# Optimization experiments

Measured on AMD Instinct MI355X. Metric: run time of the kernel, lower is better.

The kernel has to match this reference:

```python
import jax, jax.numpy as jnp
import numpy as np
import math

B, L, H, D, V, N = 16, 2048, 768, 64, 32128, 20


def setup_inputs() -> dict:
    key = jax.random.key(0)
    ks = jax.random.split(key, 10)
    f = lambda k, shape, s: jax.random.normal(k, shape, dtype=jnp.float32) * s
    return {
        "relevance": jax.random.uniform(ks[0], (B,), dtype=jnp.float32),
        "input_ids": jax.random.randint(ks[1], (B, L), 0, V),
        "wte_weight": f(ks[2], (V, H), 0.02),
        "prompts": f(ks[3], (N, H), 1.0),
        "label_prompts": f(ks[4], (2, H), 1.0),
        "aq_w": f(ks[5], (D, H), 0.02), "aq_b": jnp.zeros((D,), jnp.float32),
        "ak_w": f(ks[6], (D, H), 0.02), "ak_b": jnp.zeros((D,), jnp.float32),
        "lq_w": f(ks[7], (D, H), 0.02), "lq_b": jnp.zeros((D,), jnp.float32),
        "lk_w": f(ks[8], (D, H), 0.02), "lk_b": jnp.zeros((D,), jnp.float32),
    }


def _adapter(hidden, prompts, qw, qb, kw, kb):
    # InstanceWisePrompt: mean_L(Q K^T) == Q @ mean_L(K) (exact linearity of mean)
    Q = prompts @ qw.T + qb                    # (N, d)
    K_mean = (hidden @ kw.T + kb).mean(axis=1)  # (B, d)
    scores = jnp.einsum('nd,bd->bn', Q, K_mean) / math.sqrt(Q.shape[-1])  # (B, N)
    probs = jax.nn.sigmoid(scores)
    return prompts[None, :, :] * probs[:, :, None]  # (B, N, H)


def reference(relevance, input_ids, wte_weight, prompts, label_prompts,
              aq_w, aq_b, ak_w, ak_b, lq_w, lq_b, lk_w, lk_b):
    hs_src = wte_weight[input_ids]                       # (B, L, H) embedding gather
    rel2 = jnp.stack([1.0 - relevance, relevance], 1)    # (B, 2)
    hs_rel = (rel2 @ label_prompts)[:, None, :]          # (B, 1, H)
    lbl_prompts = _adapter(hs_rel, prompts, lq_w, lq_b, lk_w, lk_b)  # (B, N, H)
    doc_prompts = _adapter(hs_src, prompts, aq_w, aq_b, ak_w, ak_b)  # (B, N, H)
    return jnp.concatenate([lbl_prompts, doc_prompts, hs_src], axis=1)  # (B, 2N+L, H)
```

## Files before the change

kernel.cpp:

```cpp
#include <hip/hip_runtime.h>
#include <math.h>

namespace {
constexpr int B = 16, L = 2048, H = 768, D = 64, N = 20;
constexpr int TOK = 2 * N + L;
constexpr int ROWS = 16;
constexpr int NQ = N * D;
constexpr int NK = B * D;
constexpr int NQK = 2 * NQ + 2 * NK;
constexpr int WS_HSUM = 0;
constexpr int WS_QK = B * H;
constexpr int WS_PL = WS_QK + NQK;
constexpr int WS_PA = WS_PL + B * N;
}

__global__ __launch_bounds__(192) void gather_kernel(
    const int* __restrict__ ids, const float* __restrict__ wte,
    float* __restrict__ out, float* __restrict__ hsum)
{
    const int blk = blockIdx.x;
    const int b = blk / (L / ROWS);
    const int l0 = (blk % (L / ROWS)) * ROWS;
    const int t = threadIdx.x;
    float4 acc = make_float4(0.f, 0.f, 0.f, 0.f);
    float* outb = out + (size_t)b * TOK * H + (size_t)(2 * N + l0) * H;
#pragma unroll 4
    for (int r = 0; r < ROWS; ++r) {
        const int idx = ids[b * L + l0 + r];
        const float4 v = *reinterpret_cast<const float4*>(wte + (size_t)idx * H + 4 * t);
        acc.x += v.x; acc.y += v.y; acc.z += v.z; acc.w += v.w;
        *reinterpret_cast<float4*>(outb + (size_t)r * H + 4 * t) = v;
    }
    float* hs = hsum + b * H + 4 * t;
    atomicAdd(hs + 0, acc.x);
    atomicAdd(hs + 1, acc.y);
    atomicAdd(hs + 2, acc.z);
    atomicAdd(hs + 3, acc.w);
}

__global__ __launch_bounds__(256) void qk_kernel(
    const float* __restrict__ relevance, const float* __restrict__ prompts,
    const float* __restrict__ label_prompts,
    const float* __restrict__ aq_w, const float* __restrict__ aq_b,
    const float* __restrict__ ak_w, const float* __restrict__ ak_b,
    const float* __restrict__ lq_w, const float* __restrict__ lq_b,
    const float* __restrict__ lk_w, const float* __restrict__ lk_b,
    const float* __restrict__ hsum, float* __restrict__ qk)
{
    const int wave = (blockIdx.x * 256 + threadIdx.x) >> 6;
    const int lane = threadIdx.x & 63;
    if (wave >= NQK) return;

    float s = 0.f;
    float bias = 0.f;
    if (wave < NQ) {
        const int n = wave / D, d = wave % D;
        const float* x = prompts + n * H;
        const float* w = lq_w + d * H;
        for (int h = lane; h < H; h += 64) s += x[h] * w[h];
        bias = lq_b[d];
    } else if (wave < 2 * NQ) {
        const int e = wave - NQ;
        const int n = e / D, d = e % D;
        const float* x = prompts + n * H;
        const float* w = aq_w + d * H;
        for (int h = lane; h < H; h += 64) s += x[h] * w[h];
        bias = aq_b[d];
    } else if (wave < 2 * NQ + NK) {
        const int e = wave - 2 * NQ;
        const int b = e / D, d = e % D;
        const float r = relevance[b];
        const float* w = lk_w + d * H;
        for (int h = lane; h < H; h += 64) {
            const float hr = (1.f - r) * label_prompts[h] + r * label_prompts[H + h];
            s += hr * w[h];
        }
        bias = lk_b[d];
    } else {
        const int e = wave - 2 * NQ - NK;
        const int b = e / D, d = e % D;
        const float* x = hsum + b * H;
        const float* w = ak_w + d * H;
        const float inv_l = 1.f / (float)L;
        for (int h = lane; h < H; h += 64) s += (x[h] * inv_l) * w[h];
        bias = ak_b[d];
    }
#pragma unroll
    for (int off = 32; off > 0; off >>= 1) s += __shfl_xor(s, off);
    if (lane == 0) qk[wave] = s + bias;
}

__global__ __launch_bounds__(64) void score_kernel(
    const float* __restrict__ qk, float* __restrict__ probs_l,
    float* __restrict__ probs_a)
{
    const int t = blockIdx.x * 64 + threadIdx.x;
    if (t >= 2 * B * N) return;
    const int seg = t / (B * N);
    const int r = t % (B * N);
    const int b = r / N, n = r % N;
    const float* Q = qk + (seg ? NQ : 0) + n * D;
    const float* K = qk + 2 * NQ + (seg ? NK : 0) + b * D;
    float s = 0.f;
#pragma unroll
    for (int d = 0; d < D; ++d) s += Q[d] * K[d];
    s *= 0.125f;
    const float p = 1.f / (1.f + expf(-s));
    (seg ? probs_a : probs_l)[r] = p;
}

__global__ __launch_bounds__(192) void prompt_out_kernel(
    const float* __restrict__ prompts, const float* __restrict__ probs_l,
    const float* __restrict__ probs_a, float* __restrict__ out)
{
    const int blk = blockIdx.x;
    const int b = blk / (2 * N);
    const int sn = blk % (2 * N);
    const int seg = sn / N;
    const int n = sn % N;
    const float p = seg ? probs_a[b * N + n] : probs_l[b * N + n];
    const int t = threadIdx.x;
    float4 v = *reinterpret_cast<const float4*>(prompts + n * H + 4 * t);
    v.x *= p; v.y *= p; v.z *= p; v.w *= p;
    *reinterpret_cast<float4*>(out + (size_t)b * TOK * H + (size_t)sn * H + 4 * t) = v;
}

extern "C" void kernel_launch(void* const* d_in, const int* in_sizes, int n_in,
                              void* d_out, int out_size, void* d_ws, size_t ws_size,
                              hipStream_t stream)
{
    const float* relevance     = (const float*)d_in[0];
    const int*   input_ids     = (const int*)d_in[1];
    const float* wte_weight    = (const float*)d_in[2];
    const float* prompts       = (const float*)d_in[3];
    const float* label_prompts = (const float*)d_in[4];
    const float* aq_w = (const float*)d_in[5];
    const float* aq_b = (const float*)d_in[6];
    const float* ak_w = (const float*)d_in[7];
    const float* ak_b = (const float*)d_in[8];
    const float* lq_w = (const float*)d_in[9];
    const float* lq_b = (const float*)d_in[10];
    const float* lk_w = (const float*)d_in[11];
    const float* lk_b = (const float*)d_in[12];
    float* out = (float*)d_out;

    float* ws      = (float*)d_ws;
    float* hsum    = ws + WS_HSUM;
    float* qk      = ws + WS_QK;
    float* probs_l = ws + WS_PL;
    float* probs_a = ws + WS_PA;

    hipMemsetAsync(hsum, 0, B * H * sizeof(float), stream);

    gather_kernel<<<B * L / ROWS, 192, 0, stream>>>(input_ids, wte_weight, out, hsum);
    qk_kernel<<<(NQK * 64 + 255) / 256, 256, 0, stream>>>(
        relevance, prompts, label_prompts, aq_w, aq_b, ak_w, ak_b,
        lq_w, lq_b, lk_w, lk_b, hsum, qk);
    score_kernel<<<(2 * B * N + 63) / 64, 64, 0, stream>>>(qk, probs_l, probs_a);
    prompt_out_kernel<<<B * 2 * N, 192, 0, stream>>>(prompts, probs_l, probs_a, out);
}
```

Before: 236.0 us.

## Replace atomic row-sum accumulation with per-block partials and a reduce kernel

```diff
diff --git a/kernel.cpp b/kernel.cpp
--- a/kernel.cpp
+++ b/kernel.cpp
@@ -5,22 +5,25 @@
 constexpr int B = 16, L = 2048, H = 768, D = 64, N = 20;
 constexpr int TOK = 2 * N + L;
 constexpr int ROWS = 16;
+constexpr int BLK_PER_B = L / ROWS;
+constexpr int NBLK = B * BLK_PER_B;
 constexpr int NQ = N * D;
 constexpr int NK = B * D;
 constexpr int NQK = 2 * NQ + 2 * NK;
-constexpr int WS_HSUM = 0;
-constexpr int WS_QK = B * H;
-constexpr int WS_PL = WS_QK + NQK;
-constexpr int WS_PA = WS_PL + B * N;
+constexpr int WS_PART = 0;
+constexpr int WS_HSUM = NBLK * H;
+constexpr int WS_QK   = WS_HSUM + B * H;
+constexpr int WS_PL   = WS_QK + NQK;
+constexpr int WS_PA   = WS_PL + B * N;
 }
 
 __global__ __launch_bounds__(192) void gather_kernel(
     const int* __restrict__ ids, const float* __restrict__ wte,
-    float* __restrict__ out, float* __restrict__ hsum)
+    float* __restrict__ out, float* __restrict__ partial)
 {
     const int blk = blockIdx.x;
-    const int b = blk / (L / ROWS);
-    const int l0 = (blk % (L / ROWS)) * ROWS;
+    const int b = blk / BLK_PER_B;
+    const int l0 = (blk % BLK_PER_B) * ROWS;
     const int t = threadIdx.x;
     float4 acc = make_float4(0.f, 0.f, 0.f, 0.f);
     float* outb = out + (size_t)b * TOK * H + (size_t)(2 * N + l0) * H;
@@ -31,11 +34,20 @@
         acc.x += v.x; acc.y += v.y; acc.z += v.z; acc.w += v.w;
         *reinterpret_cast<float4*>(outb + (size_t)r * H + 4 * t) = v;
     }
-    float* hs = hsum + b * H + 4 * t;
-    atomicAdd(hs + 0, acc.x);
-    atomicAdd(hs + 1, acc.y);
-    atomicAdd(hs + 2, acc.z);
-    atomicAdd(hs + 3, acc.w);
+    *reinterpret_cast<float4*>(partial + (size_t)blk * H + 4 * t) = acc;
+}
+
+__global__ __launch_bounds__(256) void reduce_kernel(
+    const float* __restrict__ partial, float* __restrict__ hsum)
+{
+    const int g = blockIdx.x * 256 + threadIdx.x;
+    if (g >= B * H) return;
+    const int b = g / H, h = g % H;
+    const float* p = partial + (size_t)b * BLK_PER_B * H + h;
+    float s = 0.f;
+#pragma unroll 8
+    for (int k = 0; k < BLK_PER_B; ++k) s += p[(size_t)k * H];
+    hsum[g] = s;
 }
 
 __global__ __launch_bounds__(256) void qk_kernel(
@@ -53,36 +65,45 @@
 
     float s = 0.f;
     float bias = 0.f;
-    if (wave < NQ) {
-        const int n = wave / D, d = wave % D;
-        const float* x = prompts + n * H;
-        const float* w = lq_w + d * H;
-        for (int h = lane; h < H; h += 64) s += x[h] * w[h];
-        bias = lq_b[d];
-    } else if (wave < 2 * NQ) {
-        const int e = wave - NQ;
+    if (wave < 2 * NQ) {
+        const int e = wave < NQ ? wave : wave - NQ;
         const int n = e / D, d = e % D;
-        const float* x = prompts + n * H;
-        const float* w = aq_w + d * H;
-        for (int h = lane; h < H; h += 64) s += x[h] * w[h];
-        bias = aq_b[d];
+        const float4* x = reinterpret_cast<const float4*>(prompts + n * H);
+        const float4* w = reinterpret_cast<const float4*>(
+            (wave < NQ ? lq_w : aq_w) + d * H);
+#pragma unroll
+        for (int k = lane; k < H / 4; k += 64) {
+            const float4 a = x[k], c = w[k];
+            s += a.x * c.x + a.y * c.y + a.z * c.z + a.w * c.w;
+        }
+        bias = (wave < NQ ? lq_b : aq_b)[d];
     } else if (wave < 2 * NQ + NK) {
         const int e = wave - 2 * NQ;
         const int b = e / D, d = e % D;
         const float r = relevance[b];
-        const float* w = lk_w + d * H;
-        for (int h = lane; h < H; h += 64) {
-            const float hr = (1.f - r) * label_prompts[h] + r * label_prompts[H + h];
-            s += hr * w[h];
+        const float4* p0 = reinterpret_cast<const float4*>(label_prompts);
+        const float4* p1 = reinterpret_cast<const float4*>(label_prompts + H);
+        const float4* w = reinterpret_cast<const float4*>(lk_w + d * H);
+#pragma unroll
+        for (int k = lane; k < H / 4; k += 64) {
+            const float4 a = p0[k], bb = p1[k], c = w[k];
+            s += ((1.f - r) * a.x + r * bb.x) * c.x
+               + ((1.f - r) * a.y + r * bb.y) * c.y
+               + ((1.f - r) * a.z + r * bb.z) * c.z
+               + ((1.f - r) * a.w + r * bb.w) * c.w;
         }
         bias = lk_b[d];
     } else {
         const int e = wave - 2 * NQ - NK;
         const int b = e / D, d = e % D;
-        const float* x = hsum + b * H;
-        const float* w = ak_w + d * H;
+        const float4* x = reinterpret_cast<const float4*>(hsum + b * H);
+        const float4* w = reinterpret_cast<const float4*>(ak_w + d * H);
         const float inv_l = 1.f / (float)L;
-        for (int h = lane; h < H; h += 64) s += (x[h] * inv_l) * w[h];
+#pragma unroll
+        for (int k = lane; k < H / 4; k += 64) {
+            const float4 a = x[k], c = w[k];
+            s += inv_l * (a.x * c.x + a.y * c.y + a.z * c.z + a.w * c.w);
+        }
         bias = ak_b[d];
     }
 #pragma unroll
@@ -145,14 +166,14 @@
     float* out = (float*)d_out;
 
     float* ws      = (float*)d_ws;
+    float* partial = ws + WS_PART;
     float* hsum    = ws + WS_HSUM;
     float* qk      = ws + WS_QK;
     float* probs_l = ws + WS_PL;
     float* probs_a = ws + WS_PA;
 
-    hipMemsetAsync(hsum, 0, B * H * sizeof(float), stream);
-
-    gather_kernel<<<B * L / ROWS, 192, 0, stream>>>(input_ids, wte_weight, out, hsum);
+    gather_kernel<<<NBLK, 192, 0, stream>>>(input_ids, wte_weight, out, partial);
+    reduce_kernel<<<(B * H + 255) / 256, 256, 0, stream>>>(partial, hsum);
     qk_kernel<<<(NQK * 64 + 255) / 256, 256, 0, stream>>>(
         relevance, prompts, label_prompts, aq_w, aq_b, ak_w, ak_b,
         lq_w, lq_b, lk_w, lk_b, hsum, qk);
```

New measurement: 220.3 us. 1.07x faster.
